# Performance work log

Measured on AMD Instinct MI355X. Metric: run time of the kernel, lower is better.

The kernel has to match this reference:

```python
import jax, jax.numpy as jnp
import numpy as np

EPS = 2e-05
N_H_RDG = 9   # lifting scale grid: h_j = 2**j, j=0..8
N_H_CROP = 3  # group-conv scale support: offsets 0,1,2 (dyadic index shifts)


def _scaled_kernel(w, h):
    """Resample base kernel w [O, I, K] (taps on integers centered at 0) at
    coordinates x/h via linear interpolation -> [O, I, (K-1)*h+1], with the
    R+ Haar-measure normalization 1/h (psi_h(x) = psi(x/h)/h)."""
    K = w.shape[-1]
    Kh = (K - 1) * h + 1
    m = jnp.arange(K, dtype=jnp.float32) - K // 2
    x = (jnp.arange(Kh, dtype=jnp.float32) - Kh // 2) / h
    hat = jnp.maximum(0.0, 1.0 - jnp.abs(x[:, None] - m[None, :]))  # [Kh, K]
    return jnp.einsum('oim,xm->oix', w, hat) / h


def _conv1d_same(x, k):
    pad = (k.shape[-1] - 1) // 2
    return jax.lax.conv_general_dilated(
        x, k, window_strides=(1,), padding=[(pad, pad)],
        dimension_numbers=('NCH', 'OIH', 'NCH'))


def _pool_r1(x, stride):
    # max pool over the spatial (last) axis only: kernel 4, pad 1 each side
    return jax.lax.reduce_window(
        x, -jnp.inf, jax.lax.max,
        window_dimensions=(1, 1, 1, 4), window_strides=(1, 1, 1, stride),
        padding=((0, 0), (0, 0), (0, 0), (1, 1)))


def _bn(x, g, b):
    # BatchNorm2d over [B, C, H_scale, L], training-mode batch stats
    mu = jnp.mean(x, axis=(0, 2, 3), keepdims=True)
    var = jnp.var(x, axis=(0, 2, 3), keepdims=True)
    return (x - mu) * jax.lax.rsqrt(var + EPS) * g[None, :, None, None] + b[None, :, None, None]


def _forward(x, w1, w2, w3, g1, b1, g2, b2, g3, b3, fw1, fb1, fw2, fb2, fw3, fb3):
    B = x.shape[0]
    # --- c1: GConvRdG lifting, scales h_j = 2**j, j=0..8 ---
    out = jnp.stack([_conv1d_same(x, _scaled_kernel(w1, 2 ** j))
                     for j in range(N_H_RDG)], axis=2)      # [B,16,9,16]
    out = _bn(jax.nn.relu(_pool_r1(out, 2)), g1, b1)        # [B,16,9,8]
    # --- c2: GConvGG, h_crop=True: out scale j uses in scales j..j+2 ---
    O2, I2 = w2.shape[0], w2.shape[1]
    w2r = w2.reshape(O2, I2 * N_H_CROP, 3)
    H2 = out.shape[2] - (N_H_CROP - 1)  # 7
    out = jnp.stack([
        _conv1d_same(out[:, :, j:j + N_H_CROP, :].reshape(B, I2 * N_H_CROP, -1),
                     _scaled_kernel(w2r, 2 ** j))
        for j in range(H2)], axis=2)                        # [B,32,7,8]
    out = _bn(jax.nn.relu(_pool_r1(out, 2)), g2, b2)        # [B,32,7,4]
    # --- c3: GConvGG with 1x1 spatial kernel ---
    w3s = w3[:, :, :, 0]  # [64,32,3]
    H3 = out.shape[2] - (N_H_CROP - 1)  # 5
    out = jnp.stack([
        jnp.einsum('oik,bikl->bol', w3s, out[:, :, j:j + N_H_CROP, :]) / (2.0 ** j)
        for j in range(H3)], axis=2)                        # [B,64,5,4]
    out = _bn(jax.nn.relu(_pool_r1(out, 4)), g3, b3)        # [B,64,5,1]
    # --- MLP head (dropout is identity in eval) ---
    out = out.reshape(B, -1)                                # [B,320]
    out = out @ fw1.T + fb1
    out = out @ fw2.T + fb2
    return out @ fw3.T + fb3                                # [B,17]


def setup_inputs() -> dict:
    key = jax.random.key(0)
    ks = jax.random.split(key, 7)
    B = 4096
    x = jax.random.normal(ks[0], (B, 6, 16), dtype=jnp.float32)
    w1 = jax.random.normal(ks[1], (16, 6, 7), dtype=jnp.float32) * (6 * 7) ** -0.5
    w2 = jax.random.normal(ks[2], (32, 16, 3, 3), dtype=jnp.float32) * (16 * 3 * 3) ** -0.5
    w3 = jax.random.normal(ks[3], (64, 32, 3, 1), dtype=jnp.float32) * (32 * 3) ** -0.5
    fw1 = jax.random.normal(ks[4], (16, 320), dtype=jnp.float32) * 320 ** -0.5
    fw2 = jax.random.normal(ks[5], (16, 16), dtype=jnp.float32) * 16 ** -0.5
    fw3 = jax.random.normal(ks[6], (17, 16), dtype=jnp.float32) * 16 ** -0.5
    return {
        'x': x, 'w1': w1, 'w2': w2, 'w3': w3,
        'g1': jnp.ones(16), 'b1': jnp.zeros(16),
        'g2': jnp.ones(32), 'b2': jnp.zeros(32),
        'g3': jnp.ones(64), 'b3': jnp.zeros(64),
        'fw1': fw1, 'fb1': jnp.zeros(16),
        'fw2': fw2, 'fb2': jnp.zeros(16),
        'fw3': fw3, 'fb3': jnp.zeros(17),
    }


def reference(x, w1, w2, w3, g1, b1, g2, b2, g3, b3, fw1, fb1, fw2, fb2, fw3, fb3):
    return _forward(x, w1, w2, w3, g1, b1, g2, b2, g3, b3, fw1, fb1, fw2, fb2, fw3, fb3)
```

## Files before the change

kernel.cpp:

```cpp
#include <hip/hip_runtime.h>

#define EPS 2e-5f

using short8  = __attribute__((ext_vector_type(8))) short;
using floatx4 = __attribute__((ext_vector_type(4))) float;

static __device__ inline unsigned short f2bf(float f) {
    unsigned u = __float_as_uint(f);
    u += 0x7fffu + ((u >> 16) & 1u);
    return (unsigned short)(u >> 16);
}
static __device__ inline float bf2f(short s) {
    return __uint_as_float(((unsigned)(unsigned short)s) << 16);
}
static __device__ inline short8 scale8(short8 v, float sc) {
    short8 r;
    #pragma unroll
    for (int e = 0; e < 8; ++e) r[e] = (short)f2bf(bf2f(v[e]) * sc);
    return r;
}


__global__ void __launch_bounds__(256) kS(const float* __restrict__ w1,
                                          const float* __restrict__ w2,
                                          unsigned short* __restrict__ W1f,
                                          unsigned short* __restrict__ W2r,
                                          float* __restrict__ S,
                                          float* __restrict__ stats) {
    int gid = blockIdx.x * 256 + threadIdx.x;
    if (gid < 256) stats[gid] = 0.f;
    if (gid < 221184) {
        int j  = gid / 24576;
        int r  = gid % 24576;
        int T  = r / 1536;
        int r2 = r % 1536;
        int ks = r2 / 512;
        int r3 = r2 % 512;
        int ln = r3 >> 3, e = r3 & 7;
        int n  = T * 16 + (ln & 15);
        int kk = ks * 32 + (ln >> 4) * 8 + e;
        int o = n >> 4, t = n & 15;
        int i = kk >> 4, s = kk & 15;
        int h = 1 << j;
        int d = s - t;
        float val = 0.f;
        if (d >= -3 * h && d <= 3 * h) {
            float df = (float)d / (float)h;
            #pragma unroll
            for (int m = 0; m < 7; ++m) {
                float hat = fmaxf(0.f, 1.f - fabsf(df - (float)(m - 3)));
                val += w1[(o * 6 + i) * 7 + m] * hat;
            }
            val /= (float)h;
        }
        W1f[gid] = f2bf(val);
    } else if (gid < 909312) {
        int g  = gid - 221184;
        int fs = g >> 9;
        int ln = (g >> 3) & 63, e = g & 7;
        int j  = fs / 192;
        int rm = fs % 192;
        int T  = rm / 12, ks = rm % 12;
        int col = T * 16 + (ln & 15);
        int k   = ks * 32 + (ln >> 4) * 8 + e;
        int o = col >> 3, t = col & 7;
        int ic = k >> 3, s = k & 7;
        int i = ic / 3, c = ic % 3;
        int h = 1 << j;
        int d = s - t;
        float raw = 0.f;
        if (d >= -h && d <= h) {
            float df = (float)d / (float)h;
            #pragma unroll
            for (int m = 0; m < 3; ++m) {
                float hat = fmaxf(0.f, 1.f - fabsf(df - (float)(m - 1)));
                raw += w2[((o * 16 + i) * 3 + c) * 3 + m] * hat;
            }
            raw /= (float)h;
        }
        W2r[g] = f2bf(raw);
    } else if (gid < 937984) {
        int g = gid - 909312;
        int j = g >> 12;
        int r = g & 4095;
        int i = r >> 8;
        int col = r & 255;
        int o = col >> 3, t = col & 7;
        int h = 1 << j;
        float acc = 0.f;
        #pragma unroll
        for (int c = 0; c < 3; ++c) {
            const float* wr = &w2[((o * 16 + i) * 3 + c) * 3];
            #pragma unroll
            for (int s = 0; s < 8; ++s) {
                int d = s - t;
                if (d >= -h && d <= h) {
                    float df = (float)d / (float)h;
                    float raw = 0.f;
                    #pragma unroll
                    for (int m = 0; m < 3; ++m) {
                        float hat = fmaxf(0.f, 1.f - fabsf(df - (float)(m - 1)));
                        raw += wr[m] * hat;
                    }
                    acc += raw / (float)h;
                }
            }
        }
        S[g] = acc;
    }
}

__global__ void __launch_bounds__(256) k1(const float* __restrict__ x,
                                          const unsigned short* __restrict__ W1f,
                                          unsigned short* __restrict__ p1,
                                          float* __restrict__ stats1, int B) {
    __shared__ float z[32 * 276];
    __shared__ float lsS[256], lsQ[256];
    int tid = threadIdx.x, j = blockIdx.y;
    int wav = tid >> 6, lane = tid & 63;
    int quad = lane >> 4, l15 = lane & 15;
    int msub = wav & 1, nh = wav >> 1;
    int b0 = blockIdx.x * 32;
    floatx4 acc[8];
    #pragma unroll
    for (int T = 0; T < 8; ++T) acc[T] = floatx4{0.f, 0.f, 0.f, 0.f};
    const float* xr = x + (size_t)(b0 + msub * 16 + l15) * 96;
    const short8* Bj = (const short8*)W1f + (size_t)(j * 16) * 3 * 64;
    #pragma unroll
    for (int ks = 0; ks < 3; ++ks) {
        int k0 = ks * 32 + quad * 8;
        floatx4 v0 = *(const floatx4*)(xr + k0);
        floatx4 v1 = *(const floatx4*)(xr + k0 + 4);
        short8 a;
        #pragma unroll
        for (int e = 0; e < 4; ++e) {
            a[e]     = (short)f2bf(v0[e]);
            a[e + 4] = (short)f2bf(v1[e]);
        }
        #pragma unroll
        for (int T = 0; T < 8; ++T) {
            short8 b = Bj[((nh * 8 + T) * 3 + ks) * 64 + lane];
            acc[T] = __builtin_amdgcn_mfma_f32_16x16x32_bf16(a, b, acc[T], 0, 0, 0);
        }
    }
    #pragma unroll
    for (int T = 0; T < 8; ++T) {
        int col = (nh * 8 + T) * 16 + l15;
        int rb  = msub * 16 + quad * 4;
        #pragma unroll
        for (int r = 0; r < 4; ++r) z[(rb + r) * 276 + col] = acc[T][r];
    }
    __syncthreads();
    float psum = 0.f, pss = 0.f;
    #pragma unroll
    for (int i = 0; i < 2; ++i) {
        int u = tid + 256 * i;
        int row = u >> 4, o = u & 15;
        const float* zr = &z[row * 276 + o * 16];
        floatx4 q0 = ((const floatx4*)zr)[0];
        floatx4 q1 = ((const floatx4*)zr)[1];
        floatx4 q2 = ((const floatx4*)zr)[2];
        floatx4 q3 = ((const floatx4*)zr)[3];
        float t[16] = {q0[0], q0[1], q0[2], q0[3], q1[0], q1[1], q1[2], q1[3],
                       q2[0], q2[1], q2[2], q2[3], q3[0], q3[1], q3[2], q3[3]};
        short8 pk;
        #pragma unroll
        for (int tp = 0; tp < 8; ++tp) {
            int lo = (tp == 0) ? 0 : 2 * tp - 1;
            int hi = (tp == 7) ? 15 : 2 * tp + 2;
            float m = t[lo];
            for (int tt = lo + 1; tt <= hi; ++tt) m = fmaxf(m, t[tt]);
            m = fmaxf(m, 0.f);
            pk[tp] = (short)f2bf(m);
            psum += m; pss += m * m;
        }
        *(short8*)(p1 + ((size_t)j * B + b0 + row) * 128 + o * 8) = pk;
    }
    lsS[(tid & 15) * 16 + (tid >> 4)] = psum;
    lsQ[(tid & 15) * 16 + (tid >> 4)] = pss;
    __syncthreads();
    if (tid < 32) {
        int o = tid & 15;
        const float* src = (tid < 16) ? lsS : lsQ;
        float s = 0.f;
        #pragma unroll
        for (int g = 0; g < 16; ++g) s += src[o * 16 + g];
        atomicAdd(&stats1[(tid < 16 ? 0 : 16) + o], s);
    }
}

__global__ void __launch_bounds__(256) k2(const unsigned short* __restrict__ p1,
                                          const unsigned short* __restrict__ W2r,
                                          const float* __restrict__ S,
                                          const float* __restrict__ g1,
                                          const float* __restrict__ b1,
                                          const float* __restrict__ stats1,
                                          unsigned short* __restrict__ p2s,
                                          float* __restrict__ stats2,
                                          float invN1, int B) {
    __shared__ float z[32 * 260];
    __shared__ unsigned short pt[4][64][40];
    __shared__ float lsS[512], lsQ[512];
    __shared__ float a1s[16], d1s[16], bias2L[256];
    int tid = threadIdx.x, j = blockIdx.y;
    int wav = tid >> 6, lane = tid & 63;
    int quad = lane >> 4, l15 = lane & 15;
    int nh = wav & 1, mp = wav >> 1;
    int b0 = blockIdx.x * 64, m0 = b0 + mp * 32;
    if (tid < 16) {
        float mu  = stats1[tid] * invN1;
        float var = stats1[16 + tid] * invN1 - mu * mu;
        float rs  = rsqrtf(var + EPS);
        a1s[tid] = g1[tid] * rs;
        d1s[tid] = b1[tid] - mu * a1s[tid];
    }
    __syncthreads();
    {
        float s = 0.f;
        const float* Sj = S + (size_t)j * 4096;
        #pragma unroll
        for (int i = 0; i < 16; ++i) s = fmaf(d1s[i], Sj[i * 256 + tid], s);
        bias2L[tid] = s;
    }
    __syncthreads();
    float biasv[8];
    #pragma unroll
    for (int T = 0; T < 8; ++T) biasv[T] = bias2L[(nh * 8 + T) * 16 + l15];
    floatx4 acc[2][8];
    #pragma unroll
    for (int mi = 0; mi < 2; ++mi)
        #pragma unroll
        for (int T = 0; T < 8; ++T) acc[mi][T] = floatx4{0.f, 0.f, 0.f, 0.f};
    const short8* Bj = (const short8*)W2r + (size_t)(j * 16) * 12 * 64;
    #pragma unroll
    for (int ks = 0; ks < 12; ++ks) {
        int icq = ks * 4 + quad;
        int i = icq / 3, c = icq - i * 3;
        float a1v = a1s[i];
        const unsigned short* ap = p1 + ((size_t)(j + c) * B + m0 + l15) * 128 + i * 8;
        short8 a0 = scale8(*(const short8*)ap, a1v);
        short8 a1 = scale8(*(const short8*)(ap + 2048), a1v);
        #pragma unroll
        for (int T = 0; T < 8; ++T) {
            short8 b = Bj[((nh * 8 + T) * 12 + ks) * 64 + lane];
            acc[0][T] = __builtin_amdgcn_mfma_f32_16x16x32_bf16(a0, b, acc[0][T], 0, 0, 0);
            acc[1][T] = __builtin_amdgcn_mfma_f32_16x16x32_bf16(a1, b, acc[1][T], 0, 0, 0);
        }
    }
    float psum[2] = {0.f, 0.f}, pss[2] = {0.f, 0.f};
    for (int pass = 0; pass < 2; ++pass) {
        __syncthreads();
        if (mp == pass) {
            #pragma unroll
            for (int T = 0; T < 8; ++T) {
                int col = (nh * 8 + T) * 16 + l15;
                #pragma unroll
                for (int mi = 0; mi < 2; ++mi) {
                    int rb = mi * 16 + quad * 4;
                    #pragma unroll
                    for (int r = 0; r < 4; ++r)
                        z[(rb + r) * 260 + col] = acc[mi][T][r] + biasv[T];
                }
            }
        }
        __syncthreads();
        #pragma unroll
        for (int i2 = 0; i2 < 2; ++i2) {
            int u = tid + 256 * i2;
            int opr = u & 15, row = u >> 4;
            const float* zr = &z[row * 260 + opr * 16];
            floatx4 q0 = ((const floatx4*)zr)[0];
            floatx4 q1 = ((const floatx4*)zr)[1];
            floatx4 q2 = ((const floatx4*)zr)[2];
            floatx4 q3 = ((const floatx4*)zr)[3];
            float ta[8] = {q0[0], q0[1], q0[2], q0[3], q1[0], q1[1], q1[2], q1[3]};
            float tb[8] = {q2[0], q2[1], q2[2], q2[3], q3[0], q3[1], q3[2], q3[3]};
            int rowg = pass * 32 + row;
            #pragma unroll
            for (int tp = 0; tp < 4; ++tp) {
                int lo = (tp == 0) ? 0 : 2 * tp - 1;
                int hi = (tp == 3) ? 7 : 2 * tp + 2;
                float m0v = ta[lo], m1v = tb[lo];
                for (int tt = lo + 1; tt <= hi; ++tt) {
                    m0v = fmaxf(m0v, ta[tt]); m1v = fmaxf(m1v, tb[tt]);
                }
                m0v = fmaxf(m0v, 0.f); m1v = fmaxf(m1v, 0.f);
                psum[0] += m0v; pss[0] += m0v * m0v;
                psum[1] += m1v; pss[1] += m1v * m1v;
                unsigned pk = (unsigned)f2bf(m0v) | ((unsigned)f2bf(m1v) << 16);
                *(unsigned*)&pt[tp][rowg][opr * 2] = pk;
            }
        }
    }
    {
        int o0 = 2 * (tid & 15), g = tid >> 4;
        lsS[o0 * 16 + g] = psum[0]; lsS[(o0 + 1) * 16 + g] = psum[1];
        lsQ[o0 * 16 + g] = pss[0];  lsQ[(o0 + 1) * 16 + g] = pss[1];
    }
    __syncthreads();
    #pragma unroll
    for (int tp = 0; tp < 4; ++tp) {
        int oct = tid & 3, row = (tid >> 2) & 63;
        *(short8*)(p2s + ((size_t)(j * 4 + tp) * B + b0 + row) * 32 + oct * 8) =
            *(const short8*)&pt[tp][row][oct * 8];
    }
    if (tid < 64) {
        int o = tid & 31;
        const float* src = (tid < 32) ? lsS : lsQ;
        float s = 0.f;
        #pragma unroll
        for (int g = 0; g < 16; ++g) s += src[o * 16 + g];
        atomicAdd(&stats2[(tid < 32 ? 0 : 32) + o], s);
    }
}

__global__ void __launch_bounds__(256) k3(const unsigned short* __restrict__ p2s,
                                          const float* __restrict__ w3,
                                          const float* __restrict__ g2,
                                          const float* __restrict__ b2,
                                          const float* __restrict__ stats2,
                                          unsigned short* __restrict__ act3,
                                          float* __restrict__ stats3,
                                          float invN2, int B) {
    __shared__ float w3s[6144];
    __shared__ float a2s[32], d2s[32];
    __shared__ unsigned short atile[32][72];
    __shared__ float lsS[1024], lsQ[1024];
    int tid = threadIdx.x, j = blockIdx.y, b0 = blockIdx.x * 32;
    int og = tid >> 6, lane = tid & 63;
    int quad = lane >> 4, l15 = lane & 15;
    #pragma unroll
    for (int u = 0; u < 6; ++u) {
        int idx = tid * 4 + u * 1024;
        *(floatx4*)&w3s[idx] = *(const floatx4*)&w3[idx];
    }
    if (tid < 32) {
        float mu  = stats2[tid] * invN2;
        float var = stats2[32 + tid] * invN2 - mu * mu;
        float rs  = rsqrtf(var + EPS);
        a2s[tid] = g2[tid] * rs;
        d2s[tid] = b2[tid] - mu * a2s[tid];
    }
    __syncthreads();
    int o = og * 16 + l15;
    float biasacc = 0.f;
    short8 af[3];
    #pragma unroll
    for (int kf = 0; kf < 3; ++kf) {
        short8 v;
        #pragma unroll
        for (int e = 0; e < 8; ++e) {
            int i = quad * 8 + e;
            float raw = w3s[o * 96 + i * 3 + kf];
            v[e] = (short)f2bf(raw * a2s[i]);
            biasacc = fmaf(raw, d2s[i], biasacc);
        }
        af[kf] = v;
    }
    biasacc += __shfl_xor(biasacc, 16, 64);
    biasacc += __shfl_xor(biasacc, 32, 64);
    float brow[4];
    #pragma unroll
    for (int r = 0; r < 4; ++r) brow[r] = __shfl(biasacc, quad * 4 + r, 64);
    float inv = 1.f / (float)(1 << j);
    float psum[4] = {0.f, 0.f, 0.f, 0.f}, pss[4] = {0.f, 0.f, 0.f, 0.f};
    #pragma unroll
    for (int bt = 0; bt < 2; ++bt) {
        int bb = b0 + bt * 16;
        floatx4 aL0 = {0.f, 0.f, 0.f, 0.f};
        floatx4 aL1 = {0.f, 0.f, 0.f, 0.f};
        floatx4 aL2 = {0.f, 0.f, 0.f, 0.f};
        #pragma unroll
        for (int c = 0; c < 3; ++c) {
            const unsigned short* base =
                p2s + ((size_t)((j + c) * 4) * B + bb + l15) * 32 + quad * 8;
            short8 f0 = *(const short8*)base;
            short8 f1 = *(const short8*)(base + (size_t)B * 32);
            short8 f2v = *(const short8*)(base + (size_t)2 * B * 32);
            aL0 = __builtin_amdgcn_mfma_f32_16x16x32_bf16(af[c], f0, aL0, 0, 0, 0);
            aL1 = __builtin_amdgcn_mfma_f32_16x16x32_bf16(af[c], f1, aL1, 0, 0, 0);
            aL2 = __builtin_amdgcn_mfma_f32_16x16x32_bf16(af[c], f2v, aL2, 0, 0, 0);
        }
        #pragma unroll
        for (int r = 0; r < 4; ++r) {
            float vm = fmaxf(fmaxf(aL0[r], aL1[r]), aL2[r]);
            float v  = fmaxf((vm + brow[r]) * inv, 0.f);
            atile[bt * 16 + l15][og * 16 + quad * 4 + r] = f2bf(v);
            psum[r] += v; pss[r] += v * v;
        }
    }
    #pragma unroll
    for (int r = 0; r < 4; ++r) {
        lsS[(og * 16 + quad * 4 + r) * 16 + l15] = psum[r];
        lsQ[(og * 16 + quad * 4 + r) * 16 + l15] = pss[r];
    }
    __syncthreads();
    {
        int row = tid >> 3, oct = tid & 7;
        *(short8*)(act3 + ((size_t)j * B + b0 + row) * 64 + oct * 8) =
            *(const short8*)&atile[row][oct * 8];
    }
    if (tid < 128) {
        int oo = tid & 63;
        const float* src = (tid < 64) ? lsS : lsQ;
        float s = 0.f;
        #pragma unroll
        for (int g = 0; g < 16; ++g) s += src[oo * 16 + g];
        atomicAdd(&stats3[(tid < 64 ? 0 : 64) + oo], s);
    }
}

__global__ void __launch_bounds__(128) k4(const unsigned short* __restrict__ act3,
                                          const float* __restrict__ g3,
                                          const float* __restrict__ b3,
                                          const float* __restrict__ stats3,
                                          const float* __restrict__ fw1,
                                          const float* __restrict__ fb1,
                                          const float* __restrict__ fw2,
                                          const float* __restrict__ fb2,
                                          const float* __restrict__ fw3,
                                          const float* __restrict__ fb3,
                                          float* __restrict__ out,
                                          float invN3, int B) {
    __shared__ float fw1L[5120];
    __shared__ float a3s[64], d3s[64];
    __shared__ unsigned short W1s[5120];
    __shared__ float fw2s[256], fw3s[272], fb2s[16], fb3s[17], fb1f[16], tmp[4][16];
    __shared__ float hbuf[2][16][17];
    int tid = threadIdx.x;
    int wav = tid >> 6, lane = tid & 63;
    int quad = lane >> 4, l15 = lane & 15;
    #pragma unroll
    for (int u = 0; u < 10; ++u) {
        int idx = (tid + u * 128) * 4;
        *(floatx4*)&fw1L[idx] = *(const floatx4*)&fw1[idx];
    }
    if (tid < 64) {
        float mu  = stats3[tid] * invN3;
        float var = stats3[64 + tid] * invN3 - mu * mu;
        float rs  = rsqrtf(var + EPS);
        a3s[tid] = g3[tid] * rs;
        d3s[tid] = b3[tid] - mu * a3s[tid];
    }
    if (tid < 16) fb2s[tid] = fb2[tid];
    if (tid < 17) fb3s[tid] = fb3[tid];
    #pragma unroll
    for (int u = 0; u < 2; ++u) fw2s[tid + u * 128] = fw2[tid + u * 128];
    for (int idx = tid; idx < 272; idx += 128) fw3s[idx] = fw3[idx];
    __syncthreads();
    #pragma unroll
    for (int u = 0; u < 40; ++u) {
        int idx = tid + u * 128;
        int e  = idx & 7;
        int ln = (idx >> 3) & 63;
        int fs = idx >> 9;
        int jj = fs >> 1, ks = fs & 1;
        int n = ln & 15;
        int oo = ks * 32 + (ln >> 4) * 8 + e;
        W1s[idx] = f2bf(fw1L[n * 320 + oo * 5 + jj] * a3s[oo]);
    }
    if (tid < 64) {
        int f = tid & 15, ch = tid >> 4;
        float s = 0.f;
        for (int u = 0; u < 80; ++u) {
            int n = ch * 80 + u;
            s = fmaf(fw1L[f * 320 + n], d3s[n / 5], s);
        }
        tmp[ch][f] = s;
    }
    __syncthreads();
    if (tid < 16) fb1f[tid] = fb1[tid] + tmp[0][tid] + tmp[1][tid] + tmp[2][tid] + tmp[3][tid];
    __syncthreads();
    int mt = blockIdx.x * 2 + wav;
    floatx4 acc = {0.f, 0.f, 0.f, 0.f};
    #pragma unroll
    for (int jj = 0; jj < 5; ++jj)
        #pragma unroll
        for (int ks = 0; ks < 2; ++ks) {
            short8 a = *(const short8*)(act3 +
                ((size_t)jj * B + mt * 16 + l15) * 64 + ks * 32 + quad * 8);
            short8 b = *(const short8*)&W1s[((jj * 2 + ks) * 64 + lane) * 8];
            acc = __builtin_amdgcn_mfma_f32_16x16x32_bf16(a, b, acc, 0, 0, 0);
        }
    #pragma unroll
    for (int r = 0; r < 4; ++r) hbuf[wav][quad * 4 + r][l15] = acc[r] + fb1f[l15];
    __syncthreads();
    if (lane < 16) {
        int row = l15;
        float hv[16];
        #pragma unroll
        for (int n = 0; n < 16; ++n) hv[n] = hbuf[wav][row][n];
        float h2[16];
        #pragma unroll
        for (int f2 = 0; f2 < 16; ++f2) {
            float s = fb2s[f2];
            #pragma unroll
            for (int n = 0; n < 16; ++n) s = fmaf(fw2s[f2 * 16 + n], hv[n], s);
            h2[f2] = s;
        }
        float* orow = out + (size_t)(mt * 16 + row) * 17;
        #pragma unroll
        for (int f3 = 0; f3 < 17; ++f3) {
            float s = fb3s[f3];
            #pragma unroll
            for (int n = 0; n < 16; ++n) s = fmaf(fw3s[f3 * 16 + n], h2[n], s);
            orow[f3] = s;
        }
    }
}

extern "C" void kernel_launch(void* const* d_in, const int* in_sizes, int n_in,
                              void* d_out, int out_size, void* d_ws, size_t ws_size,
                              hipStream_t stream) {
    (void)n_in; (void)out_size; (void)ws_size;
    const float* x   = (const float*)d_in[0];
    const float* w1  = (const float*)d_in[1];
    const float* w2  = (const float*)d_in[2];
    const float* w3  = (const float*)d_in[3];
    const float* g1  = (const float*)d_in[4];
    const float* b1  = (const float*)d_in[5];
    const float* g2  = (const float*)d_in[6];
    const float* b2  = (const float*)d_in[7];
    const float* g3  = (const float*)d_in[8];
    const float* b3  = (const float*)d_in[9];
    const float* fw1 = (const float*)d_in[10];
    const float* fb1 = (const float*)d_in[11];
    const float* fw2 = (const float*)d_in[12];
    const float* fb2 = (const float*)d_in[13];
    const float* fw3 = (const float*)d_in[14];
    const float* fb3 = (const float*)d_in[15];
    float* out = (float*)d_out;

    int B = in_sizes[0] / 96;

    char* wsb = (char*)d_ws;
    float*          stats = (float*)wsb;
    unsigned short* W1f   = (unsigned short*)(wsb + 1024);
    unsigned short* W2r   = W1f + 221184;
    float*          S     = (float*)(W2r + 688128);
    unsigned short* p1    = (unsigned short*)(S + 28672);
    unsigned short* p2s   = p1 + (size_t)9 * B * 128;
    unsigned short* act3  = p2s + (size_t)28 * B * 32;

    float* stats1 = stats;
    float* stats2 = stats + 32;
    float* stats3 = stats + 96;

    float invN1 = 1.f / (float)(B * 72);
    float invN2 = 1.f / (float)(B * 28);
    float invN3 = 1.f / (float)(B * 5);

    kS<<<3665, 256, 0, stream>>>(w1, w2, W1f, W2r, S, stats);
    k1<<<dim3(B / 32, 9), 256, 0, stream>>>(x, W1f, p1, stats1, B);
    k2<<<dim3(B / 64, 7), 256, 0, stream>>>(p1, W2r, S, g1, b1, stats1, p2s, stats2,
                                            invN1, B);
    k3<<<dim3(B / 32, 5), 256, 0, stream>>>(p2s, w3, g2, b2, stats2, act3, stats3,
                                            invN2, B);
    k4<<<B / 32, 128, 0, stream>>>(act3, g3, b3, stats3, fw1, fb1, fw2, fb2, fw3, fb3,
                                   out, invN3, B);
}
```

Measured before the change: 173.2 us.

## Fuse all stages into one persistent cooperative kernel with grid syncs

```diff
diff --git a/kernel.cpp b/kernel.cpp
--- a/kernel.cpp
+++ b/kernel.cpp
@@ -1,4 +1,7 @@
 #include <hip/hip_runtime.h>
+#include <hip/hip_cooperative_groups.h>
+
+namespace cg = cooperative_groups;
 
 #define EPS 2e-5f
 
@@ -18,6 +21,511 @@
     #pragma unroll
     for (int e = 0; e < 8; ++e) r[e] = (short)f2bf(bf2f(v[e]) * sc);
     return r;
+}
+
+
+struct ShP1 {
+    float z[32 * 276];
+    float lsS[256], lsQ[256];
+};
+struct ShP2 {
+    float z[32 * 260];
+    unsigned short pt[4][64][40];
+    float lsS[512], lsQ[512];
+    float a1s[16], d1s[16], bias2L[256];
+};
+struct ShP3 {
+    float w3s[6144];
+    float a2s[32], d2s[32];
+    unsigned short atile[32][72];
+    float lsS[1024], lsQ[1024];
+};
+struct ShP4 {
+    float fw1L[5120];
+    float a3s[64], d3s[64];
+    unsigned short W1s[5120];
+    float fw2s[256], fw3s[272], fb2s[16], fb3s[17], fb1f[16], tmp[4][16];
+    float hbuf[4][16][17];
+};
+union ShU { ShP1 s1; ShP2 s2; ShP3 s3; ShP4 s4; };
+
+__global__ void __launch_bounds__(256, 2)
+fused(const float* __restrict__ x,  const float* __restrict__ w1,
+      const float* __restrict__ w2, const float* __restrict__ w3,
+      const float* __restrict__ g1, const float* __restrict__ b1,
+      const float* __restrict__ g2, const float* __restrict__ b2,
+      const float* __restrict__ g3, const float* __restrict__ b3,
+      const float* __restrict__ fw1, const float* __restrict__ fb1,
+      const float* __restrict__ fw2, const float* __restrict__ fb2,
+      const float* __restrict__ fw3, const float* __restrict__ fb3,
+      float* __restrict__ out,
+      unsigned short* __restrict__ W1f, unsigned short* __restrict__ W2r,
+      float* __restrict__ S,
+      unsigned short* __restrict__ p1, unsigned short* __restrict__ p2s,
+      unsigned short* __restrict__ act3, float* __restrict__ stats,
+      float invN1, float invN2, float invN3, int B) {
+    cg::grid_group gg = cg::this_grid();
+    __shared__ ShU sh;
+    const int tid = threadIdx.x;
+    const int bid = blockIdx.x;
+    const int G   = gridDim.x;
+    float* stats1 = stats;
+    float* stats2 = stats + 32;
+    float* stats3 = stats + 96;
+
+    for (int gid = bid * 256 + tid; gid < 937984; gid += G * 256) {
+        if (gid < 256) stats[gid] = 0.f;
+        if (gid < 221184) {
+            int j  = gid / 24576;
+            int r  = gid % 24576;
+            int T  = r / 1536;
+            int r2 = r % 1536;
+            int ks = r2 / 512;
+            int r3 = r2 % 512;
+            int ln = r3 >> 3, e = r3 & 7;
+            int n  = T * 16 + (ln & 15);
+            int kk = ks * 32 + (ln >> 4) * 8 + e;
+            int o = n >> 4, t = n & 15;
+            int i = kk >> 4, s = kk & 15;
+            int h = 1 << j;
+            int d = s - t;
+            float val = 0.f;
+            if (d >= -3 * h && d <= 3 * h) {
+                float df = (float)d / (float)h;
+                #pragma unroll
+                for (int m = 0; m < 7; ++m) {
+                    float hat = fmaxf(0.f, 1.f - fabsf(df - (float)(m - 3)));
+                    val += w1[(o * 6 + i) * 7 + m] * hat;
+                }
+                val /= (float)h;
+            }
+            W1f[gid] = f2bf(val);
+        } else if (gid < 909312) {
+            int g  = gid - 221184;
+            int fs = g >> 9;
+            int ln = (g >> 3) & 63, e = g & 7;
+            int j  = fs / 192;
+            int rm = fs % 192;
+            int T  = rm / 12, ks = rm % 12;
+            int col = T * 16 + (ln & 15);
+            int k   = ks * 32 + (ln >> 4) * 8 + e;
+            int o = col >> 3, t = col & 7;
+            int ic = k >> 3, s = k & 7;
+            int i = ic / 3, c = ic % 3;
+            int h = 1 << j;
+            int d = s - t;
+            float raw = 0.f;
+            if (d >= -h && d <= h) {
+                float df = (float)d / (float)h;
+                #pragma unroll
+                for (int m = 0; m < 3; ++m) {
+                    float hat = fmaxf(0.f, 1.f - fabsf(df - (float)(m - 1)));
+                    raw += w2[((o * 16 + i) * 3 + c) * 3 + m] * hat;
+                }
+                raw /= (float)h;
+            }
+            W2r[g] = f2bf(raw);
+        } else {
+            int g = gid - 909312;
+            int j = g >> 12;
+            int r = g & 4095;
+            int i = r >> 8;
+            int col = r & 255;
+            int o = col >> 3, t = col & 7;
+            int h = 1 << j;
+            float acc = 0.f;
+            #pragma unroll
+            for (int c = 0; c < 3; ++c) {
+                const float* wr = &w2[((o * 16 + i) * 3 + c) * 3];
+                #pragma unroll
+                for (int s = 0; s < 8; ++s) {
+                    int d = s - t;
+                    if (d >= -h && d <= h) {
+                        float df = (float)d / (float)h;
+                        float raw = 0.f;
+                        #pragma unroll
+                        for (int m = 0; m < 3; ++m) {
+                            float hat = fmaxf(0.f, 1.f - fabsf(df - (float)(m - 1)));
+                            raw += wr[m] * hat;
+                        }
+                        acc += raw / (float)h;
+                    }
+                }
+            }
+            S[g] = acc;
+        }
+    }
+    gg.sync();
+
+    {
+        const int wav = tid >> 6, lane = tid & 63;
+        const int quad = lane >> 4, l15 = lane & 15;
+        const int msub = wav & 1, nh = wav >> 1;
+        const int nb1 = B / 32;
+        for (int t = bid; t < nb1 * 9; t += G) {
+            int j1 = t / nb1, bxx = t - j1 * nb1;
+            int b0 = bxx * 32;
+            __syncthreads();
+            floatx4 acc[8];
+            #pragma unroll
+            for (int T = 0; T < 8; ++T) acc[T] = floatx4{0.f, 0.f, 0.f, 0.f};
+            const float* xr = x + (size_t)(b0 + msub * 16 + l15) * 96;
+            const short8* Bj = (const short8*)W1f + (size_t)(j1 * 16) * 3 * 64;
+            #pragma unroll
+            for (int ks = 0; ks < 3; ++ks) {
+                int k0 = ks * 32 + quad * 8;
+                floatx4 v0 = *(const floatx4*)(xr + k0);
+                floatx4 v1 = *(const floatx4*)(xr + k0 + 4);
+                short8 a;
+                #pragma unroll
+                for (int e = 0; e < 4; ++e) {
+                    a[e]     = (short)f2bf(v0[e]);
+                    a[e + 4] = (short)f2bf(v1[e]);
+                }
+                #pragma unroll
+                for (int T = 0; T < 8; ++T) {
+                    short8 b = Bj[((nh * 8 + T) * 3 + ks) * 64 + lane];
+                    acc[T] = __builtin_amdgcn_mfma_f32_16x16x32_bf16(a, b, acc[T], 0, 0, 0);
+                }
+            }
+            #pragma unroll
+            for (int T = 0; T < 8; ++T) {
+                int col = (nh * 8 + T) * 16 + l15;
+                int rb  = msub * 16 + quad * 4;
+                #pragma unroll
+                for (int r = 0; r < 4; ++r) sh.s1.z[(rb + r) * 276 + col] = acc[T][r];
+            }
+            __syncthreads();
+            float psum = 0.f, pss = 0.f;
+            #pragma unroll
+            for (int i = 0; i < 2; ++i) {
+                int u = tid + 256 * i;
+                int row = u >> 4, o = u & 15;
+                const float* zr = &sh.s1.z[row * 276 + o * 16];
+                floatx4 q0 = ((const floatx4*)zr)[0];
+                floatx4 q1 = ((const floatx4*)zr)[1];
+                floatx4 q2 = ((const floatx4*)zr)[2];
+                floatx4 q3 = ((const floatx4*)zr)[3];
+                float tt[16] = {q0[0], q0[1], q0[2], q0[3], q1[0], q1[1], q1[2], q1[3],
+                                q2[0], q2[1], q2[2], q2[3], q3[0], q3[1], q3[2], q3[3]};
+                short8 pk;
+                #pragma unroll
+                for (int tp = 0; tp < 8; ++tp) {
+                    int lo = (tp == 0) ? 0 : 2 * tp - 1;
+                    int hi = (tp == 7) ? 15 : 2 * tp + 2;
+                    float m = tt[lo];
+                    for (int t2 = lo + 1; t2 <= hi; ++t2) m = fmaxf(m, tt[t2]);
+                    m = fmaxf(m, 0.f);
+                    pk[tp] = (short)f2bf(m);
+                    psum += m; pss += m * m;
+                }
+                *(short8*)(p1 + ((size_t)j1 * B + b0 + row) * 128 + o * 8) = pk;
+            }
+            sh.s1.lsS[(tid & 15) * 16 + (tid >> 4)] = psum;
+            sh.s1.lsQ[(tid & 15) * 16 + (tid >> 4)] = pss;
+            __syncthreads();
+            if (tid < 32) {
+                int o = tid & 15;
+                const float* src = (tid < 16) ? sh.s1.lsS : sh.s1.lsQ;
+                float s = 0.f;
+                #pragma unroll
+                for (int g = 0; g < 16; ++g) s += src[o * 16 + g];
+                atomicAdd(&stats1[(tid < 16 ? 0 : 16) + o], s);
+            }
+        }
+    }
+    gg.sync();
+
+    {
+        const int wav = tid >> 6, lane = tid & 63;
+        const int quad = lane >> 4, l15 = lane & 15;
+        const int nh = wav & 1, mp = wav >> 1;
+        if (tid < 16) {
+            float mu  = stats1[tid] * invN1;
+            float var = stats1[16 + tid] * invN1 - mu * mu;
+            float rs  = rsqrtf(var + EPS);
+            sh.s2.a1s[tid] = g1[tid] * rs;
+            sh.s2.d1s[tid] = b1[tid] - mu * sh.s2.a1s[tid];
+        }
+        const int nb2 = B / 64;
+        for (int t = bid; t < nb2 * 7; t += G) {
+            int j2 = t / nb2, bxx = t - j2 * nb2;
+            int b0 = bxx * 64, m0 = b0 + mp * 32;
+            __syncthreads();
+            {
+                float s = 0.f;
+                const float* Sj = S + (size_t)j2 * 4096;
+                #pragma unroll
+                for (int i = 0; i < 16; ++i) s = fmaf(sh.s2.d1s[i], Sj[i * 256 + tid], s);
+                sh.s2.bias2L[tid] = s;
+            }
+            __syncthreads();
+            float biasv[8];
+            #pragma unroll
+            for (int T = 0; T < 8; ++T) biasv[T] = sh.s2.bias2L[(nh * 8 + T) * 16 + l15];
+            floatx4 acc[2][8];
+            #pragma unroll
+            for (int mi = 0; mi < 2; ++mi)
+                #pragma unroll
+                for (int T = 0; T < 8; ++T) acc[mi][T] = floatx4{0.f, 0.f, 0.f, 0.f};
+            const short8* Bj = (const short8*)W2r + (size_t)(j2 * 16) * 12 * 64;
+            #pragma unroll
+            for (int ks = 0; ks < 12; ++ks) {
+                int icq = ks * 4 + quad;
+                int i = icq / 3, c = icq - i * 3;
+                float a1v = sh.s2.a1s[i];
+                const unsigned short* ap = p1 + ((size_t)(j2 + c) * B + m0 + l15) * 128 + i * 8;
+                short8 a0 = scale8(*(const short8*)ap, a1v);
+                short8 a1 = scale8(*(const short8*)(ap + 2048), a1v);
+                #pragma unroll
+                for (int T = 0; T < 8; ++T) {
+                    short8 b = Bj[((nh * 8 + T) * 12 + ks) * 64 + lane];
+                    acc[0][T] = __builtin_amdgcn_mfma_f32_16x16x32_bf16(a0, b, acc[0][T], 0, 0, 0);
+                    acc[1][T] = __builtin_amdgcn_mfma_f32_16x16x32_bf16(a1, b, acc[1][T], 0, 0, 0);
+                }
+            }
+            float psum[2] = {0.f, 0.f}, pss[2] = {0.f, 0.f};
+            for (int pass = 0; pass < 2; ++pass) {
+                __syncthreads();
+                if (mp == pass) {
+                    #pragma unroll
+                    for (int T = 0; T < 8; ++T) {
+                        int col = (nh * 8 + T) * 16 + l15;
+                        #pragma unroll
+                        for (int mi = 0; mi < 2; ++mi) {
+                            int rb = mi * 16 + quad * 4;
+                            #pragma unroll
+                            for (int r = 0; r < 4; ++r)
+                                sh.s2.z[(rb + r) * 260 + col] = acc[mi][T][r] + biasv[T];
+                        }
+                    }
+                }
+                __syncthreads();
+                #pragma unroll
+                for (int i2 = 0; i2 < 2; ++i2) {
+                    int u = tid + 256 * i2;
+                    int opr = u & 15, row = u >> 4;
+                    const float* zr = &sh.s2.z[row * 260 + opr * 16];
+                    floatx4 q0 = ((const floatx4*)zr)[0];
+                    floatx4 q1 = ((const floatx4*)zr)[1];
+                    floatx4 q2 = ((const floatx4*)zr)[2];
+                    floatx4 q3 = ((const floatx4*)zr)[3];
+                    float ta[8] = {q0[0], q0[1], q0[2], q0[3], q1[0], q1[1], q1[2], q1[3]};
+                    float tb[8] = {q2[0], q2[1], q2[2], q2[3], q3[0], q3[1], q3[2], q3[3]};
+                    int rowg = pass * 32 + row;
+                    #pragma unroll
+                    for (int tp = 0; tp < 4; ++tp) {
+                        int lo = (tp == 0) ? 0 : 2 * tp - 1;
+                        int hi = (tp == 3) ? 7 : 2 * tp + 2;
+                        float m0v = ta[lo], m1v = tb[lo];
+                        for (int t2 = lo + 1; t2 <= hi; ++t2) {
+                            m0v = fmaxf(m0v, ta[t2]); m1v = fmaxf(m1v, tb[t2]);
+                        }
+                        m0v = fmaxf(m0v, 0.f); m1v = fmaxf(m1v, 0.f);
+                        psum[0] += m0v; pss[0] += m0v * m0v;
+                        psum[1] += m1v; pss[1] += m1v * m1v;
+                        unsigned pk = (unsigned)f2bf(m0v) | ((unsigned)f2bf(m1v) << 16);
+                        *(unsigned*)&sh.s2.pt[tp][rowg][opr * 2] = pk;
+                    }
+                }
+            }
+            {
+                int o0 = 2 * (tid & 15), g = tid >> 4;
+                sh.s2.lsS[o0 * 16 + g] = psum[0]; sh.s2.lsS[(o0 + 1) * 16 + g] = psum[1];
+                sh.s2.lsQ[o0 * 16 + g] = pss[0];  sh.s2.lsQ[(o0 + 1) * 16 + g] = pss[1];
+            }
+            __syncthreads();
+            #pragma unroll
+            for (int tp = 0; tp < 4; ++tp) {
+                int oct = tid & 3, row = (tid >> 2) & 63;
+                *(short8*)(p2s + ((size_t)(j2 * 4 + tp) * B + b0 + row) * 32 + oct * 8) =
+                    *(const short8*)&sh.s2.pt[tp][row][oct * 8];
+            }
+            if (tid < 64) {
+                int o = tid & 31;
+                const float* src = (tid < 32) ? sh.s2.lsS : sh.s2.lsQ;
+                float s = 0.f;
+                #pragma unroll
+                for (int g = 0; g < 16; ++g) s += src[o * 16 + g];
+                atomicAdd(&stats2[(tid < 32 ? 0 : 32) + o], s);
+            }
+        }
+    }
+    gg.sync();
+
+    {
+        const int og = tid >> 6, lane = tid & 63;
+        const int quad = lane >> 4, l15 = lane & 15;
+        #pragma unroll
+        for (int u = 0; u < 6; ++u) {
+            int idx = tid * 4 + u * 1024;
+            *(floatx4*)&sh.s3.w3s[idx] = *(const floatx4*)&w3[idx];
+        }
+        if (tid < 32) {
+            float mu  = stats2[tid] * invN2;
+            float var = stats2[32 + tid] * invN2 - mu * mu;
+            float rs  = rsqrtf(var + EPS);
+            sh.s3.a2s[tid] = g2[tid] * rs;
+            sh.s3.d2s[tid] = b2[tid] - mu * sh.s3.a2s[tid];
+        }
+        __syncthreads();
+        int o = og * 16 + l15;
+        float biasacc = 0.f;
+        short8 af[3];
+        #pragma unroll
+        for (int kf = 0; kf < 3; ++kf) {
+            short8 v;
+            #pragma unroll
+            for (int e = 0; e < 8; ++e) {
+                int i = quad * 8 + e;
+                float raw = sh.s3.w3s[o * 96 + i * 3 + kf];
+                v[e] = (short)f2bf(raw * sh.s3.a2s[i]);
+                biasacc = fmaf(raw, sh.s3.d2s[i], biasacc);
+            }
+            af[kf] = v;
+        }
+        biasacc += __shfl_xor(biasacc, 16, 64);
+        biasacc += __shfl_xor(biasacc, 32, 64);
+        float brow[4];
+        #pragma unroll
+        for (int r = 0; r < 4; ++r) brow[r] = __shfl(biasacc, quad * 4 + r, 64);
+        const int nb3 = B / 32;
+        for (int t = bid; t < nb3 * 5; t += G) {
+            int j3 = t / nb3, bxx = t - j3 * nb3;
+            int b0 = bxx * 32;
+            float inv = 1.f / (float)(1 << j3);
+            __syncthreads();
+            float psum[4] = {0.f, 0.f, 0.f, 0.f}, pss[4] = {0.f, 0.f, 0.f, 0.f};
+            #pragma unroll
+            for (int bt = 0; bt < 2; ++bt) {
+                int bb = b0 + bt * 16;
+                floatx4 aL0 = {0.f, 0.f, 0.f, 0.f};
+                floatx4 aL1 = {0.f, 0.f, 0.f, 0.f};
+                floatx4 aL2 = {0.f, 0.f, 0.f, 0.f};
+                #pragma unroll
+                for (int c = 0; c < 3; ++c) {
+                    const unsigned short* base =
+                        p2s + ((size_t)((j3 + c) * 4) * B + bb + l15) * 32 + quad * 8;
+                    short8 f0 = *(const short8*)base;
+                    short8 f1 = *(const short8*)(base + (size_t)B * 32);
+                    short8 f2v = *(const short8*)(base + (size_t)2 * B * 32);
+                    aL0 = __builtin_amdgcn_mfma_f32_16x16x32_bf16(af[c], f0, aL0, 0, 0, 0);
+                    aL1 = __builtin_amdgcn_mfma_f32_16x16x32_bf16(af[c], f1, aL1, 0, 0, 0);
+                    aL2 = __builtin_amdgcn_mfma_f32_16x16x32_bf16(af[c], f2v, aL2, 0, 0, 0);
+                }
+                #pragma unroll
+                for (int r = 0; r < 4; ++r) {
+                    float vm = fmaxf(fmaxf(aL0[r], aL1[r]), aL2[r]);
+                    float v  = fmaxf((vm + brow[r]) * inv, 0.f);
+                    sh.s3.atile[bt * 16 + l15][og * 16 + quad * 4 + r] = f2bf(v);
+                    psum[r] += v; pss[r] += v * v;
+                }
+            }
+            #pragma unroll
+            for (int r = 0; r < 4; ++r) {
+                sh.s3.lsS[(og * 16 + quad * 4 + r) * 16 + l15] = psum[r];
+                sh.s3.lsQ[(og * 16 + quad * 4 + r) * 16 + l15] = pss[r];
+            }
+            __syncthreads();
+            {
+                int row = tid >> 3, oct = tid & 7;
+                *(short8*)(act3 + ((size_t)j3 * B + b0 + row) * 64 + oct * 8) =
+                    *(const short8*)&sh.s3.atile[row][oct * 8];
+            }
+            if (tid < 128) {
+                int oo = tid & 63;
+                const float* src = (tid < 64) ? sh.s3.lsS : sh.s3.lsQ;
+                float s = 0.f;
+                #pragma unroll
+                for (int g = 0; g < 16; ++g) s += src[oo * 16 + g];
+                atomicAdd(&stats3[(tid < 64 ? 0 : 64) + oo], s);
+            }
+        }
+    }
+    gg.sync();
+
+    if (bid < B / 64) {
+        const int wav = tid >> 6, lane = tid & 63;
+        const int quad = lane >> 4, l15 = lane & 15;
+        #pragma unroll
+        for (int u = 0; u < 5; ++u) {
+            int idx = (tid + u * 256) * 4;
+            *(floatx4*)&sh.s4.fw1L[idx] = *(const floatx4*)&fw1[idx];
+        }
+        if (tid < 64) {
+            float mu  = stats3[tid] * invN3;
+            float var = stats3[64 + tid] * invN3 - mu * mu;
+            float rs  = rsqrtf(var + EPS);
+            sh.s4.a3s[tid] = g3[tid] * rs;
+            sh.s4.d3s[tid] = b3[tid] - mu * sh.s4.a3s[tid];
+        }
+        if (tid < 16) sh.s4.fb2s[tid] = fb2[tid];
+        if (tid < 17) sh.s4.fb3s[tid] = fb3[tid];
+        sh.s4.fw2s[tid] = fw2[tid];
+        for (int idx = tid; idx < 272; idx += 256) sh.s4.fw3s[idx] = fw3[idx];
+        __syncthreads();
+        #pragma unroll
+        for (int u = 0; u < 20; ++u) {
+            int idx = tid + u * 256;
+            int e  = idx & 7;
+            int ln = (idx >> 3) & 63;
+            int fs = idx >> 9;
+            int jj = fs >> 1, ks = fs & 1;
+            int n = ln & 15;
+            int oo = ks * 32 + (ln >> 4) * 8 + e;
+            sh.s4.W1s[idx] = f2bf(sh.s4.fw1L[n * 320 + oo * 5 + jj] * sh.s4.a3s[oo]);
+        }
+        if (tid < 64) {
+            int f = tid & 15, ch = tid >> 4;
+            float s = 0.f;
+            for (int u = 0; u < 80; ++u) {
+                int n = ch * 80 + u;
+                s = fmaf(sh.s4.fw1L[f * 320 + n], sh.s4.d3s[n / 5], s);
+            }
+            sh.s4.tmp[ch][f] = s;
+        }
+        __syncthreads();
+        if (tid < 16) sh.s4.fb1f[tid] = fb1[tid] + sh.s4.tmp[0][tid] + sh.s4.tmp[1][tid]
+                                      + sh.s4.tmp[2][tid] + sh.s4.tmp[3][tid];
+        __syncthreads();
+        int mt = bid * 4 + wav;
+        floatx4 acc = {0.f, 0.f, 0.f, 0.f};
+        #pragma unroll
+        for (int jj = 0; jj < 5; ++jj)
+            #pragma unroll
+            for (int ks = 0; ks < 2; ++ks) {
+                short8 a = *(const short8*)(act3 +
+                    ((size_t)jj * B + mt * 16 + l15) * 64 + ks * 32 + quad * 8);
+                short8 b = *(const short8*)&sh.s4.W1s[((jj * 2 + ks) * 64 + lane) * 8];
+                acc = __builtin_amdgcn_mfma_f32_16x16x32_bf16(a, b, acc, 0, 0, 0);
+            }
+        #pragma unroll
+        for (int r = 0; r < 4; ++r)
+            sh.s4.hbuf[wav][quad * 4 + r][l15] = acc[r] + sh.s4.fb1f[l15];
+        __syncthreads();
+        if (lane < 16) {
+            int row = l15;
+            float hv[16];
+            #pragma unroll
+            for (int n = 0; n < 16; ++n) hv[n] = sh.s4.hbuf[wav][row][n];
+            float h2[16];
+            #pragma unroll
+            for (int f2 = 0; f2 < 16; ++f2) {
+                float s = sh.s4.fb2s[f2];
+                #pragma unroll
+                for (int n = 0; n < 16; ++n) s = fmaf(sh.s4.fw2s[f2 * 16 + n], hv[n], s);
+                h2[f2] = s;
+            }
+            float* orow = out + (size_t)(mt * 16 + row) * 17;
+            #pragma unroll
+            for (int f3 = 0; f3 < 17; ++f3) {
+                float s = sh.s4.fb3s[f3];
+                #pragma unroll
+                for (int n = 0; n < 16; ++n) s = fmaf(sh.s4.fw3s[f3 * 16 + n], h2[n], s);
+                orow[f3] = s;
+            }
+        }
+    }
 }
 
 
@@ -550,12 +1058,46 @@
     float invN2 = 1.f / (float)(B * 28);
     float invN3 = 1.f / (float)(B * 5);
 
-    kS<<<3665, 256, 0, stream>>>(w1, w2, W1f, W2r, S, stats);
-    k1<<<dim3(B / 32, 9), 256, 0, stream>>>(x, W1f, p1, stats1, B);
-    k2<<<dim3(B / 64, 7), 256, 0, stream>>>(p1, W2r, S, g1, b1, stats1, p2s, stats2,
-                                            invN1, B);
-    k3<<<dim3(B / 32, 5), 256, 0, stream>>>(p2s, w3, g2, b2, stats2, act3, stats3,
-                                            invN2, B);
-    k4<<<B / 32, 128, 0, stream>>>(act3, g3, b3, stats3, fw1, fb1, fw2, fb2, fw3, fb3,
-                                   out, invN3, B);
+    static int coopGrid = -2;
+    if (coopGrid == -2) {
+        int nb = 0;
+        hipError_t e = hipOccupancyMaxActiveBlocksPerMultiprocessor(&nb, fused, 256, 0);
+        if (e == hipSuccess && nb > 0) {
+            long g = (long)nb * 256;
+            if (g > 1152) g = 1152;
+            coopGrid = (int)g;
+        } else {
+            coopGrid = -1;
+            (void)hipGetLastError();
+        }
+    }
+    bool launched = false;
+    if (coopGrid > 0) {
+        void* args[] = {
+            (void*)&x,   (void*)&w1,  (void*)&w2,  (void*)&w3,
+            (void*)&g1,  (void*)&b1,  (void*)&g2,  (void*)&b2,
+            (void*)&g3,  (void*)&b3,  (void*)&fw1, (void*)&fb1,
+            (void*)&fw2, (void*)&fb2, (void*)&fw3, (void*)&fb3,
+            (void*)&out, (void*)&W1f, (void*)&W2r, (void*)&S,
+            (void*)&p1,  (void*)&p2s, (void*)&act3, (void*)&stats,
+            (void*)&invN1, (void*)&invN2, (void*)&invN3, (void*)&B };
+        hipError_t e = hipLaunchCooperativeKernel((const void*)fused, dim3(coopGrid),
+                                                  dim3(256), args, 0, stream);
+        if (e == hipSuccess) {
+            launched = true;
+        } else {
+            coopGrid = -1;
+            (void)hipGetLastError();
+        }
+    }
+    if (!launched) {
+        kS<<<3665, 256, 0, stream>>>(w1, w2, W1f, W2r, S, stats);
+        k1<<<dim3(B / 32, 9), 256, 0, stream>>>(x, W1f, p1, stats1, B);
+        k2<<<dim3(B / 64, 7), 256, 0, stream>>>(p1, W2r, S, g1, b1, stats1, p2s, stats2,
+                                                invN1, B);
+        k3<<<dim3(B / 32, 5), 256, 0, stream>>>(p2s, w3, g2, b2, stats2, act3, stats3,
+                                                invN2, B);
+        k4<<<B / 32, 128, 0, stream>>>(act3, g3, b3, stats3, fw1, fb1, fw2, fb2, fw3, fb3,
+                                       out, invN3, B);
+    }
 }
```

Result: slower. 339.3 us (+95.9%).
